# Optimization experiments

Measured on AMD Instinct MI355X. Metric: run time of the kernel, lower is better.

## Reference

```python
import jax, jax.numpy as jnp
import numpy as np

EMB = 1024
HEADS = 16
HEAD_DIM = EMB // HEADS
B, T = 2, 2048
EPS = 1e-5


def setup_inputs() -> dict:
    key = jax.random.key(0)
    ks = jax.random.split(key, 12)
    s_in = (1.0 / np.sqrt(EMB)).astype(np.float32)
    s_hid = (1.0 / np.sqrt(4 * EMB)).astype(np.float32)
    return {
        "x": jax.random.normal(ks[0], (B, T, EMB), jnp.float32),
        "Wq": jax.random.normal(ks[1], (HEADS, EMB, HEAD_DIM), jnp.float32) * s_in,
        "Wk": jax.random.normal(ks[2], (HEADS, EMB, HEAD_DIM), jnp.float32) * s_in,
        "Wv": jax.random.normal(ks[3], (HEADS, EMB, HEAD_DIM), jnp.float32) * s_in,
        "W1": jax.random.normal(ks[4], (EMB, 4 * EMB), jnp.float32) * s_in,
        "b1": jnp.zeros((4 * EMB,), jnp.float32),
        "W2": jax.random.normal(ks[5], (4 * EMB, EMB), jnp.float32) * s_hid,
        "b2": jnp.zeros((EMB,), jnp.float32),
        "g1": jnp.ones((EMB,), jnp.float32),
        "be1": jnp.zeros((EMB,), jnp.float32),
        "g2": jnp.ones((EMB,), jnp.float32),
        "be2": jnp.zeros((EMB,), jnp.float32),
    }


def _layernorm1d(x, gain, bias):
    # Faithful to source: normalize over dim 1 (sequence dim of [B,T,C]),
    # with UNBIASED variance (torch.var default).
    mean = jnp.mean(x, axis=1, keepdims=True)
    var = jnp.var(x, axis=1, keepdims=True, ddof=1)
    return gain * (x - mean) / jnp.sqrt(var + EPS) + bias


def _attention(x, Wq, Wk, Wv):
    Bq, Tq, C = x.shape
    q = jnp.einsum("btc,hcd->bhtd", x, Wq)
    k = jnp.einsum("btc,hcd->bhtd", x, Wk)
    v = jnp.einsum("btc,hcd->bhtd", x, Wv)
    # NOTE: scale uses input channel dim C (=emb_size), as in the source.
    wei = jnp.einsum("bhtd,bhsd->bhts", q, k) * (C ** -0.5)
    causal = jnp.tril(jnp.ones((Tq, Tq), bool))
    wei = jnp.where(causal, wei, -jnp.inf)
    wei = jax.nn.softmax(wei, axis=-1)
    out = jnp.einsum("bhts,bhsd->bhtd", wei, v)
    # concat over heads (dim=-1) == transpose + reshape
    return out.transpose(0, 2, 1, 3).reshape(Bq, Tq, -1)


def reference(x, Wq, Wk, Wv, W1, b1, W2, b2, g1, be1, g2, be2):
    x = x + _attention(_layernorm1d(x, g1, be1), Wq, Wk, Wv)
    h = _layernorm1d(x, g2, be2)
    h = jax.nn.relu(h @ W1 + b1) @ W2 + b2
    return x + h
```

## Files before the change

kernel.cpp:

```cpp
#include <hip/hip_runtime.h>


typedef __bf16 bf16x8 __attribute__((ext_vector_type(8)));
typedef float f32x4 __attribute__((ext_vector_type(4)));
typedef unsigned short u16;
typedef u16 u16x8 __attribute__((ext_vector_type(8)));
typedef u16 u16x4 __attribute__((ext_vector_type(4)));

#define MFMA16 __builtin_amdgcn_mfma_f32_16x16x32_bf16

__device__ __forceinline__ u16 f2bf(float f) {
  return __builtin_bit_cast(u16, (__bf16)f);
}
__device__ __forceinline__ float bf2f(u16 u) {
  return __builtin_bit_cast(float, (unsigned)u << 16);
}
__device__ __forceinline__ bf16x8 ldbf8(const u16* p) {
  return __builtin_bit_cast(bf16x8, *reinterpret_cast<const u16x8*>(p));
}
__device__ __forceinline__ void gll16(const void* g, void* l) {
  __builtin_amdgcn_global_load_lds((const __attribute__((address_space(1))) void*)g,
                                   (__attribute__((address_space(3))) void*)l, 16, 0, 0);
}
template <int N>
__device__ __forceinline__ void wait_vm() {
  if constexpr (N == 0)      asm volatile("s_waitcnt vmcnt(0)" ::: "memory");
  else if constexpr (N == 6) asm volatile("s_waitcnt vmcnt(6)" ::: "memory");
  else if constexpr (N == 8) asm volatile("s_waitcnt vmcnt(8)" ::: "memory");
  else                       asm volatile("s_waitcnt vmcnt(16)" ::: "memory");
}
__device__ __forceinline__ void barrier_raw() {
  asm volatile("" ::: "memory");
  __builtin_amdgcn_s_barrier();
  asm volatile("" ::: "memory");
}
__device__ __forceinline__ int qb_off(int qb) {
  if (qb < 8)  return qb;
  if (qb < 16) return 8 + (qb - 8) * 2;
  if (qb < 24) return 24 + (qb - 16) * 3;
  return 48 + (qb - 24) * 4;
}

__global__ __launch_bounds__(256) void transpose_big2(const float* __restrict__ W1,
                                                      const float* __restrict__ W2,
                                                      u16* __restrict__ o1,
                                                      u16* __restrict__ o2) {
  __shared__ float tile[64][65];
  int id = blockIdx.x;
  const float* in;
  u16* out;
  int K, N, kb, nb;
  if (id < 1024) { in = W1; out = o1; K = 1024; N = 4096; kb = id & 15; nb = id >> 4; }
  else { id -= 1024; in = W2; out = o2; K = 4096; N = 1024; kb = id >> 4; nb = id & 15; }
  const int k0 = kb * 64, n0 = nb * 64;
  const int c = threadIdx.x & 63, rg = threadIdx.x >> 6;
#pragma unroll
  for (int i = 0; i < 16; ++i) {
    int r = rg * 16 + i;
    tile[r][c] = in[(size_t)(k0 + r) * N + n0 + c];
  }
  __syncthreads();
#pragma unroll
  for (int i = 0; i < 16; ++i) {
    int nl = rg * 16 + i;
    out[(size_t)(n0 + nl) * K + k0 + c] = f2bf(tile[c][nl]);
  }
}

__global__ __launch_bounds__(256) void transpose_head3(const float* __restrict__ Wq,
                                                       const float* __restrict__ Wk,
                                                       const float* __restrict__ Wv,
                                                       u16* __restrict__ out, float scale) {
  __shared__ float tile[64][65];
  const int z = blockIdx.z;
  const float* W = z == 0 ? Wq : (z == 1 ? Wk : Wv);
  const float sc = z == 0 ? scale : 1.0f;
  const int k0 = blockIdx.x * 64, h = blockIdx.y;
  const float* in = W + (size_t)h * 1024 * 64;
  const int c = threadIdx.x & 63, rg = threadIdx.x >> 6;
#pragma unroll
  for (int i = 0; i < 16; ++i) {
    int r = rg * 16 + i;
    tile[r][c] = in[(size_t)(k0 + r) * 64 + c];
  }
  __syncthreads();
#pragma unroll
  for (int i = 0; i < 16; ++i) {
    int nl = rg * 16 + i;
    out[(size_t)(z * 1024 + h * 64 + nl) * 1024 + k0 + c] = f2bf(tile[c][nl] * sc);
  }
}

__global__ __launch_bounds__(256) void ln_partial(const float* __restrict__ x,
                                                  float2* __restrict__ part) {
  const int b = blockIdx.x >> 4, c0 = (blockIdx.x & 15) * 64;
  const int c = c0 + (threadIdx.x & 63), tg = threadIdx.x >> 6;
  const int t0 = blockIdx.y * 256 + tg * 64;
  float s = 0.f, sq = 0.f;
  const float* p = x + (size_t)(b * 2048 + t0) * 1024 + c;
#pragma unroll 8
  for (int i = 0; i < 64; ++i) {
    float v = p[(size_t)i * 1024];
    s += v; sq += v * v;
  }
  __shared__ float ss[256], sb[256];
  ss[threadIdx.x] = s; sb[threadIdx.x] = sq;
  __syncthreads();
  if (threadIdx.x < 64) {
    s  = ss[threadIdx.x] + ss[threadIdx.x + 64] + ss[threadIdx.x + 128] + ss[threadIdx.x + 192];
    sq = sb[threadIdx.x] + sb[threadIdx.x + 64] + sb[threadIdx.x + 128] + sb[threadIdx.x + 192];
    part[(size_t)(b * 1024 + c) * 8 + blockIdx.y] = make_float2(s, sq);
  }
}

template <int NC>
__global__ __launch_bounds__(256) void ln_stats(const float2* __restrict__ part,
                                                float2* __restrict__ stats) {
  const int bc = blockIdx.x * 256 + threadIdx.x;
  float s = 0.f, sq = 0.f;
#pragma unroll
  for (int i = 0; i < NC; ++i) {
    float2 v = part[(size_t)bc * NC + i];
    s += v.x; sq += v.y;
  }
  const float mean = s * (1.0f / 2048.0f);
  const float var = (sq - 2048.0f * mean * mean) * (1.0f / 2047.0f);
  stats[bc] = make_float2(mean, rsqrtf(var + 1e-5f));
}

__global__ __launch_bounds__(256) void ln_apply(const float* __restrict__ x,
                                                const float2* __restrict__ stats,
                                                const float* __restrict__ g,
                                                const float* __restrict__ be,
                                                u16* __restrict__ out) {
  const size_t flat = ((size_t)blockIdx.x * 256 + threadIdx.x) * 4;
  const int b = (int)(flat >> 21);
  const int c = (int)(flat & 1023);
  float4 xv = *reinterpret_cast<const float4*>(x + flat);
  float vs[4] = {xv.x, xv.y, xv.z, xv.w};
  u16x4 o;
#pragma unroll
  for (int j = 0; j < 4; ++j) {
    float2 st = stats[b * 1024 + c + j];
    o[j] = f2bf(g[c + j] * (vs[j] - st.x) * st.y + be[c + j]);
  }
  *reinterpret_cast<u16x4*>(out + flat) = o;
}

template <int WTN, int EPI, int MINW>
__global__ __launch_bounds__(256, MINW) void gemm_kernel(const u16* __restrict__ A,
                                                         const u16* __restrict__ Bt,
                                                         u16* __restrict__ outb,
                                                         float* __restrict__ outf,
                                                         const float* __restrict__ bias,
                                                         const float* __restrict__ resid,
                                                         int N, int K) {
  constexpr int BM = 128, BN = 2 * WTN;
  constexpr int NI = WTN / 16;
  constexpr int BCH = BN / 8;
  constexpr int LPW = (16 + BCH) / 4;
  __shared__ alignas(16) u16 sA[2][BM * 64];
  __shared__ alignas(16) u16 sB[2][BN * 64];
  const int gx = gridDim.x;
  const int nwg = gx * gridDim.y;
  int bid = blockIdx.y * gx + blockIdx.x;
  bid = (bid & 7) * (nwg >> 3) + (bid >> 3);
  const int n0 = (bid % gx) * BN, m0 = (bid / gx) * BM;
  const int tid = threadIdx.x, lane = tid & 63, wid = tid >> 6;
  const int wm = (wid >> 1) * 64, wn = (wid & 1) * WTN;
  const int lr = lane & 15, lg = lane >> 4;
  const int srow = lane >> 3;
  const int sgr = (lane & 7) ^ srow;
  const int x7 = lr & 7;
  f32x4 acc[4][NI] = {};

  auto stage = [&](int buf, int k0) {
#pragma unroll
    for (int i = 0; i < LPW; ++i) {
      const int c = wid * LPW + i;
      if (c < 16) {
        const int r = c * 8 + srow;
        gll16(A + (size_t)(m0 + r) * K + k0 + sgr * 8, &sA[buf][c * 512]);
      } else {
        const int r = (c - 16) * 8 + srow;
        gll16(Bt + (size_t)(n0 + r) * K + k0 + sgr * 8, &sB[buf][(c - 16) * 512]);
      }
    }
  };

  const int nsteps = K >> 6;
  stage(0, 0);
  int cur = 0;
  for (int t = 0; t < nsteps; ++t) {
    if (t + 1 < nsteps) {
      stage(cur ^ 1, (t + 1) * 64);
      wait_vm<LPW>();
    } else {
      wait_vm<0>();
    }
    barrier_raw();
    bf16x8 af[4][2], bfr[NI][2];
#pragma unroll
    for (int mi = 0; mi < 4; ++mi)
#pragma unroll
      for (int kk = 0; kk < 2; ++kk)
        af[mi][kk] = ldbf8(&sA[cur][(wm + mi * 16 + lr) * 64 + (((kk * 4 + lg) ^ x7) * 8)]);
#pragma unroll
    for (int ni = 0; ni < NI; ++ni)
#pragma unroll
      for (int kk = 0; kk < 2; ++kk)
        bfr[ni][kk] = ldbf8(&sB[cur][(wn + ni * 16 + lr) * 64 + (((kk * 4 + lg) ^ x7) * 8)]);
#pragma unroll
    for (int kk = 0; kk < 2; ++kk)
#pragma unroll
      for (int mi = 0; mi < 4; ++mi)
#pragma unroll
        for (int ni = 0; ni < NI; ++ni)
          acc[mi][ni] = MFMA16(af[mi][kk], bfr[ni][kk], acc[mi][ni], 0, 0, 0);
    barrier_raw();
    cur ^= 1;
  }

#pragma unroll
  for (int mi = 0; mi < 4; ++mi)
#pragma unroll
    for (int ni = 0; ni < NI; ++ni)
#pragma unroll
      for (int r = 0; r < 4; ++r) {
        const int row = m0 + wm + mi * 16 + lg * 4 + r;
        const int col = n0 + wn + ni * 16 + lr;
        float v = acc[mi][ni][r];
        if (EPI == 0) {
          outb[(size_t)row * N + col] = f2bf(v);
        } else if (EPI == 1) {
          v += bias[col];
          v = fmaxf(v, 0.f);
          outb[(size_t)row * N + col] = f2bf(v);
        } else {
          v += bias[col] + resid[(size_t)row * N + col];
          outf[(size_t)row * N + col] = v;
        }
      }
}

__global__ __launch_bounds__(256) void attn_partial(const u16* __restrict__ qk,
                                                    const u16* __restrict__ vt,
                                                    u16* __restrict__ Opart,
                                                    float2* __restrict__ ml) {
  const int xr = 79 - (int)blockIdx.x;
  int qb, ch, nc;
  if (xr < 8)       { qb = xr;                ch = 0;            nc = 1; }
  else if (xr < 24) { qb = 8 + ((xr - 8) >> 1);  ch = (xr - 8) & 1;  nc = 2; }
  else if (xr < 48) { qb = 16 + (xr - 24) / 3;   ch = (xr - 24) % 3; nc = 3; }
  else              { qb = 24 + ((xr - 48) >> 2); ch = (xr - 48) & 3; nc = 4; }
  const int nt_tot = qb + 1;
  const int t0 = (ch * nt_tot) / nc;
  const int t1 = ((ch + 1) * nt_tot) / nc;
  const int bh = blockIdx.y, b = bh >> 4, h = bh & 15;
  const int slot = bh * 80 + xr;
  const int q0 = qb * 64;
  const int tid = threadIdx.x, lane = tid & 63, w = tid >> 6;
  const int lr = lane & 15, lg = lane >> 4;
  __shared__ alignas(16) u16 sK[64 * 64];
  __shared__ alignas(16) u16 sV[64 * 64];
  __shared__ alignas(16) u16 sP[4][16 * 64];

  const size_t qrow = (size_t)(b * 2048 + q0 + w * 16 + lr) * 2048 + h * 64;
  const bf16x8 aq0 = ldbf8(qk + qrow + lg * 8);
  const bf16x8 aq1 = ldbf8(qk + qrow + 32 + lg * 8);

  float m_i[4], l_i[4];
  f32x4 acc[4];
#pragma unroll
  for (int r = 0; r < 4; ++r) { m_i[r] = -1e30f; l_i[r] = 0.f; }
#pragma unroll
  for (int dn = 0; dn < 4; ++dn) acc[dn] = f32x4{0.f, 0.f, 0.f, 0.f};

  auto stage = [&](int s0) {
#pragma unroll
    for (int i = 0; i < 2; ++i) {
      const int c = w * 2 + i;
      const int g = c * 64 + lane;
      const int row = g >> 3;
      const int cs = (g & 7) ^ (row & 7);
      gll16(qk + (size_t)(b * 2048 + s0 + row) * 2048 + 1024 + h * 64 + cs * 8,
            &sK[c * 512]);
      gll16(vt + (size_t)(h * 64 + row) * 4096 + b * 2048 + s0 + cs * 8,
            &sV[c * 512]);
    }
  };

  for (int t = t0; t < t1; ++t) {
    stage(t * 64);
    wait_vm<0>();
    barrier_raw();

    f32x4 sf[4];
    __builtin_amdgcn_s_setprio(1);
#pragma unroll
    for (int sn = 0; sn < 4; ++sn) {
      const int row = sn * 16 + lr;
      const int x7 = lr & 7;
      bf16x8 k0f = ldbf8(&sK[row * 64 + ((lg ^ x7) * 8)]);
      bf16x8 k1f = ldbf8(&sK[row * 64 + (((4 + lg) ^ x7) * 8)]);
      f32x4 z = {0.f, 0.f, 0.f, 0.f};
      z = MFMA16(aq0, k0f, z, 0, 0, 0);
      z = MFMA16(aq1, k1f, z, 0, 0, 0);
      sf[sn] = z;
    }
    __builtin_amdgcn_s_setprio(0);

    if (t == nt_tot - 1) {
      const int qlb = w * 16 + lg * 4;
#pragma unroll
      for (int sn = 0; sn < 4; ++sn)
#pragma unroll
        for (int r = 0; r < 4; ++r)
          if (sn * 16 + lr > qlb + r) sf[sn][r] = -1e30f;
    }

    float pm[4];
    bool need = false;
#pragma unroll
    for (int r = 0; r < 4; ++r) {
      pm[r] = fmaxf(fmaxf(sf[0][r], sf[1][r]), fmaxf(sf[2][r], sf[3][r]));
      need = need || (pm[r] > m_i[r] + 8.f);
    }
    if (__any(need)) {
#pragma unroll
      for (int r = 0; r < 4; ++r) {
        float mx = pm[r];
        mx = fmaxf(mx, __shfl_xor(mx, 1, 16));
        mx = fmaxf(mx, __shfl_xor(mx, 2, 16));
        mx = fmaxf(mx, __shfl_xor(mx, 4, 16));
        mx = fmaxf(mx, __shfl_xor(mx, 8, 16));
        const float mnew = fmaxf(m_i[r], mx);
        const float al = exp2f(m_i[r] - mnew);
        l_i[r] *= al;
        acc[0][r] *= al; acc[1][r] *= al; acc[2][r] *= al; acc[3][r] *= al;
        m_i[r] = mnew;
      }
    }

    const int x7p = lr & 7;
#pragma unroll
    for (int r = 0; r < 4; ++r) {
      const float p0 = exp2f(sf[0][r] - m_i[r]), p1 = exp2f(sf[1][r] - m_i[r]);
      const float p2 = exp2f(sf[2][r] - m_i[r]), p3 = exp2f(sf[3][r] - m_i[r]);
      l_i[r] += (p0 + p1) + (p2 + p3);
      const int prow = lg * 4 + r;
      const int pb = prow * 64, px = prow & 7;
      sP[w][pb + (((lr >> 3) ^ px) * 8) + (lr & 7)]       = f2bf(p0);
      sP[w][pb + (((2 + (lr >> 3)) ^ px) * 8) + (lr & 7)] = f2bf(p1);
      sP[w][pb + (((4 + (lr >> 3)) ^ px) * 8) + (lr & 7)] = f2bf(p2);
      sP[w][pb + (((6 + (lr >> 3)) ^ px) * 8) + (lr & 7)] = f2bf(p3);
    }

    const bf16x8 pa0 = ldbf8(&sP[w][lr * 64 + ((lg ^ x7p) * 8)]);
    const bf16x8 pa1 = ldbf8(&sP[w][lr * 64 + (((4 + lg) ^ x7p) * 8)]);
    __builtin_amdgcn_s_setprio(1);
#pragma unroll
    for (int dn = 0; dn < 4; ++dn) {
      const int row = dn * 16 + lr;
      bf16x8 v0f = ldbf8(&sV[row * 64 + ((lg ^ x7p) * 8)]);
      bf16x8 v1f = ldbf8(&sV[row * 64 + (((4 + lg) ^ x7p) * 8)]);
      acc[dn] = MFMA16(pa0, v0f, acc[dn], 0, 0, 0);
      acc[dn] = MFMA16(pa1, v1f, acc[dn], 0, 0, 0);
    }
    __builtin_amdgcn_s_setprio(0);
    barrier_raw();
  }

  const int rbase = w * 16 + lg * 4;
#pragma unroll
  for (int r = 0; r < 4; ++r) {
    float ls = l_i[r];
    ls += __shfl_xor(ls, 1, 16);
    ls += __shfl_xor(ls, 2, 16);
    ls += __shfl_xor(ls, 4, 16);
    ls += __shfl_xor(ls, 8, 16);
    const int row = rbase + r;
    if (lr == 0) ml[(size_t)slot * 64 + row] = make_float2(m_i[r], ls);
#pragma unroll
    for (int dn = 0; dn < 4; ++dn)
      Opart[((size_t)slot * 64 + row) * 64 + dn * 16 + lr] = f2bf(acc[dn][r]);
  }
}

__global__ __launch_bounds__(256) void attn_merge_ln(const u16* __restrict__ Opart,
                                                     const float2* __restrict__ ml,
                                                     const float* __restrict__ x,
                                                     float* __restrict__ x2,
                                                     float2* __restrict__ part) {
  const int qb = blockIdx.x, bh = blockIdx.y, b = bh >> 4, h = bh & 15;
  const int nc = (qb >> 3) + 1;
  const size_t slot0 = (size_t)bh * 80 + qb_off(qb);
  const int tid = threadIdx.x;
  const int row = tid >> 2, d0 = (tid & 3) * 16;
  __shared__ float red[64][65];

  float wgt[4];
  float mmax = -1e30f, lsum = 0.f;
  for (int i = 0; i < nc; ++i) {
    float2 v = ml[(slot0 + i) * 64 + row];
    wgt[i] = v.x;
    mmax = fmaxf(mmax, v.x);
  }
  for (int i = 0; i < nc; ++i) {
    float2 v = ml[(slot0 + i) * 64 + row];
    wgt[i] = exp2f(wgt[i] - mmax);
    lsum += wgt[i] * v.y;
  }
  const float inv = 1.0f / lsum;

#pragma unroll
  for (int half = 0; half < 2; ++half) {
    const int d = d0 + half * 8;
    float o[8] = {0.f, 0.f, 0.f, 0.f, 0.f, 0.f, 0.f, 0.f};
    for (int i = 0; i < nc; ++i) {
      u16x8 v = *reinterpret_cast<const u16x8*>(&Opart[((slot0 + i) * 64 + row) * 64 + d]);
#pragma unroll
      for (int jj = 0; jj < 8; ++jj) o[jj] += wgt[i] * bf2f(v[jj]);
    }
    const size_t idx = ((size_t)(b * 2048 + qb * 64 + row)) * 1024 + h * 64 + d;
    float4 x0 = *reinterpret_cast<const float4*>(x + idx);
    float4 x1 = *reinterpret_cast<const float4*>(x + idx + 4);
    float4 o0 = make_float4(x0.x + o[0] * inv, x0.y + o[1] * inv, x0.z + o[2] * inv, x0.w + o[3] * inv);
    float4 o1 = make_float4(x1.x + o[4] * inv, x1.y + o[5] * inv, x1.z + o[6] * inv, x1.w + o[7] * inv);
    *reinterpret_cast<float4*>(x2 + idx) = o0;
    *reinterpret_cast<float4*>(x2 + idx + 4) = o1;
    red[row][d + 0] = o0.x; red[row][d + 1] = o0.y; red[row][d + 2] = o0.z; red[row][d + 3] = o0.w;
    red[row][d + 4] = o1.x; red[row][d + 5] = o1.y; red[row][d + 6] = o1.z; red[row][d + 7] = o1.w;
  }
  __syncthreads();
  if (tid < 64) {
    float s = 0.f, sq = 0.f;
#pragma unroll 8
    for (int t = 0; t < 64; ++t) {
      float v = red[t][tid];
      s += v; sq += v * v;
    }
    part[(size_t)(b * 1024 + h * 64 + tid) * 32 + qb] = make_float2(s, sq);
  }
}

extern "C" void kernel_launch(void* const* d_in, const int* in_sizes, int n_in,
                              void* d_out, int out_size, void* d_ws, size_t ws_size,
                              hipStream_t stream) {
  const float* x   = (const float*)d_in[0];
  const float* Wq  = (const float*)d_in[1];
  const float* Wk  = (const float*)d_in[2];
  const float* Wv  = (const float*)d_in[3];
  const float* W1  = (const float*)d_in[4];
  const float* b1  = (const float*)d_in[5];
  const float* W2  = (const float*)d_in[6];
  const float* b2  = (const float*)d_in[7];
  const float* g1  = (const float*)d_in[8];
  const float* be1 = (const float*)d_in[9];
  const float* g2  = (const float*)d_in[10];
  const float* be2 = (const float*)d_in[11];
  float* out = (float*)d_out;

  char* ws = (char*)d_ws;
  size_t off = 0;
  auto alloc = [&](size_t bytes) { char* p = ws + off; off += (bytes + 255) & ~(size_t)255; return p; };
  u16*    qkb   = (u16*)alloc(4096ull * 2048 * 2);
  u16*    vtb   = (u16*)alloc(1024ull * 4096 * 2);
  (void)alloc(4096ull * 1024 * 2);
  u16*    h1    = qkb;
  float*  x2    = (float*)alloc(4096ull * 1024 * 4);
  u16*    hbuf  = (u16*)alloc(4096ull * 1024 * 2);
  u16*    wqkvt = (u16*)alloc(3072ull * 1024 * 2);
  u16*    w1t   = (u16*)alloc(4096ull * 1024 * 2);
  u16*    w2t   = (u16*)alloc(1024ull * 4096 * 2);
  float2* part  = (float2*)alloc(2048ull * 32 * 8);
  float2* stats = (float2*)alloc(2048ull * 8);
  u16*    Opart = (u16*)alloc(32ull * 80 * 64 * 64 * 2);
  float2* ml    = (float2*)alloc(32ull * 80 * 64 * 8);
  (void)ws_size; (void)in_sizes; (void)n_in; (void)out_size;

  const float SC = 0.03125f * 1.44269504088896341f;
  transpose_head3<<<dim3(16, 16, 3), 256, 0, stream>>>(Wq, Wk, Wv, wqkvt, SC);
  transpose_big2<<<2048, 256, 0, stream>>>(W1, W2, w1t, w2t);

  ln_partial<<<dim3(32, 8), 256, 0, stream>>>(x, part);
  ln_stats<8><<<8, 256, 0, stream>>>(part, stats);
  ln_apply<<<4096, 256, 0, stream>>>(x, stats, g1, be1, hbuf);

  gemm_kernel<64, 0, 2><<<dim3(16, 32), 256, 0, stream>>>(hbuf, wqkvt, qkb, nullptr, nullptr, nullptr, 2048, 1024);
  gemm_kernel<32, 0, 3><<<dim3(64, 8), 256, 0, stream>>>(wqkvt + 2048 * 1024, hbuf, vtb, nullptr, nullptr, nullptr, 4096, 1024);

  attn_partial<<<dim3(80, 32), 256, 0, stream>>>(qkb, vtb, Opart, ml);
  attn_merge_ln<<<dim3(32, 32), 256, 0, stream>>>(Opart, ml, x, x2, part);

  ln_stats<32><<<8, 256, 0, stream>>>(part, stats);
  ln_apply<<<4096, 256, 0, stream>>>(x2, stats, g2, be2, hbuf);

  gemm_kernel<64, 1, 2><<<dim3(32, 32), 256, 0, stream>>>(hbuf, w1t, h1, nullptr, b1, nullptr, 4096, 1024);

  gemm_kernel<32, 2, 3><<<dim3(16, 32), 256, 0, stream>>>(h1, w2t, nullptr, out, b2, x2, 1024, 4096);
}
```

Baseline: 237.4 us.

## Register-prefetch next K/V tile to overlap global loads with attention compute

Replaces the direct global-to-LDS loads, which were waited on immediately, with register-staged loads. The next K/V tile is fetched into registers while the current tile is computed, then written to LDS at the start of the next iteration. This is meant to hide global memory latency behind the QK and PV MFMA work. In exchange it uses more VGPRs, which may lower occupancy, and adds explicit LDS stores plus a restructured barrier placement.

```diff
diff --git a/kernel.cpp b/kernel.cpp
--- a/kernel.cpp
+++ b/kernel.cpp
@@ -276,23 +276,32 @@
 #pragma unroll
   for (int dn = 0; dn < 4; ++dn) acc[dn] = f32x4{0.f, 0.f, 0.f, 0.f};
 
-  auto stage = [&](int s0) {
-#pragma unroll
-    for (int i = 0; i < 2; ++i) {
-      const int c = w * 2 + i;
-      const int g = c * 64 + lane;
-      const int row = g >> 3;
-      const int cs = (g & 7) ^ (row & 7);
-      gll16(qk + (size_t)(b * 2048 + s0 + row) * 2048 + 1024 + h * 64 + cs * 8,
-            &sK[c * 512]);
-      gll16(vt + (size_t)(h * 64 + row) * 4096 + b * 2048 + s0 + cs * 8,
-            &sV[c * 512]);
-    }
+  const int c0 = w * 2, c1 = w * 2 + 1;
+  const int g0 = c0 * 64 + lane, r0 = g0 >> 3, cs0 = (g0 & 7) ^ (r0 & 7);
+  const int g1 = c1 * 64 + lane, r1 = g1 >> 3, cs1 = (g1 & 7) ^ (r1 & 7);
+  const u16* kbase0 = qk + (size_t)(b * 2048 + r0) * 2048 + 1024 + h * 64 + cs0 * 8;
+  const u16* kbase1 = qk + (size_t)(b * 2048 + r1) * 2048 + 1024 + h * 64 + cs1 * 8;
+  const u16* vbase0 = vt + (size_t)(h * 64 + r0) * 4096 + b * 2048 + cs0 * 8;
+  const u16* vbase1 = vt + (size_t)(h * 64 + r1) * 4096 + b * 2048 + cs1 * 8;
+
+  u16x8 kA0, kA1, vA0, vA1, kB0, kB1, vB0, vB1;
+  auto LOAD = [&](int s0, u16x8& k0r, u16x8& k1r, u16x8& v0r, u16x8& v1r) {
+    k0r = *reinterpret_cast<const u16x8*>(kbase0 + (size_t)s0 * 2048);
+    k1r = *reinterpret_cast<const u16x8*>(kbase1 + (size_t)s0 * 2048);
+    v0r = *reinterpret_cast<const u16x8*>(vbase0 + s0);
+    v1r = *reinterpret_cast<const u16x8*>(vbase1 + s0);
   };
 
+  LOAD(t0 * 64, kA0, kA1, vA0, vA1);
+
   for (int t = t0; t < t1; ++t) {
-    stage(t * 64);
-    wait_vm<0>();
+    barrier_raw();
+    *reinterpret_cast<u16x8*>(&sK[c0 * 512 + lane * 8]) = kA0;
+    *reinterpret_cast<u16x8*>(&sK[c1 * 512 + lane * 8]) = kA1;
+    *reinterpret_cast<u16x8*>(&sV[c0 * 512 + lane * 8]) = vA0;
+    *reinterpret_cast<u16x8*>(&sV[c1 * 512 + lane * 8]) = vA1;
+    if (t + 1 < t1) LOAD((t + 1) * 64, kB0, kB1, vB0, vB1);
+    asm volatile("s_waitcnt lgkmcnt(0)" ::: "memory");
     barrier_raw();
 
     f32x4 sf[4];
@@ -368,7 +377,8 @@
       acc[dn] = MFMA16(pa1, v1f, acc[dn], 0, 0, 0);
     }
     __builtin_amdgcn_s_setprio(0);
-    barrier_raw();
+
+    kA0 = kB0; kA1 = kB1; vA0 = vB0; vA1 = vB1;
   }
 
   const int rbase = w * 16 + lg * 4;
```

Result: slower. 243.3 us (+2.5%).

## Enlarge attention query tile to 128 rows so each K/V tile serves two halves

Applied to the files above, without the earlier changes.

Each attention block now handles 128 query rows instead of 64, with each wave owning 32 rows split into two 16-row halves. Every staged K/V tile is reused across both halves, which halves global K/V traffic and barrier count per query row. The split-KV schedule, partial-output layout, merge kernel (now 512 threads, 128 rows) and LN partial count are adjusted to match. In exchange the grid has half as many attention blocks (1280 vs 2560), register use rises, and causal masking now covers the last two KV tiles.

```diff
diff --git a/kernel.cpp b/kernel.cpp
--- a/kernel.cpp
+++ b/kernel.cpp
@@ -34,11 +34,11 @@
   __builtin_amdgcn_s_barrier();
   asm volatile("" ::: "memory");
 }
-__device__ __forceinline__ int qb_off(int qb) {
-  if (qb < 8)  return qb;
-  if (qb < 16) return 8 + (qb - 8) * 2;
-  if (qb < 24) return 24 + (qb - 16) * 3;
-  return 48 + (qb - 24) * 4;
+__device__ __forceinline__ int qb_off2(int k) {
+  if (k < 4)  return k;
+  if (k < 8)  return 4 + (k - 4) * 2;
+  if (k < 12) return 12 + (k - 8) * 3;
+  return 24 + (k - 12) * 4;
 }
 
 __global__ __launch_bounds__(256) void transpose_big2(const float* __restrict__ W1,
@@ -247,34 +247,38 @@
                                                     const u16* __restrict__ vt,
                                                     u16* __restrict__ Opart,
                                                     float2* __restrict__ ml) {
-  const int xr = 79 - (int)blockIdx.x;
-  int qb, ch, nc;
-  if (xr < 8)       { qb = xr;                ch = 0;            nc = 1; }
-  else if (xr < 24) { qb = 8 + ((xr - 8) >> 1);  ch = (xr - 8) & 1;  nc = 2; }
-  else if (xr < 48) { qb = 16 + (xr - 24) / 3;   ch = (xr - 24) % 3; nc = 3; }
-  else              { qb = 24 + ((xr - 48) >> 2); ch = (xr - 48) & 3; nc = 4; }
-  const int nt_tot = qb + 1;
+  const int xr = 39 - (int)blockIdx.x;
+  int k, ch, nc;
+  if (xr < 4)       { k = xr;                 ch = 0;             nc = 1; }
+  else if (xr < 12) { k = 4 + ((xr - 4) >> 1);   ch = (xr - 4) & 1;   nc = 2; }
+  else if (xr < 24) { k = 8 + (xr - 12) / 3;    ch = (xr - 12) % 3;  nc = 3; }
+  else              { k = 12 + ((xr - 24) >> 2); ch = (xr - 24) & 3;  nc = 4; }
+  const int nt_tot = 2 * k + 2;
   const int t0 = (ch * nt_tot) / nc;
   const int t1 = ((ch + 1) * nt_tot) / nc;
   const int bh = blockIdx.y, b = bh >> 4, h = bh & 15;
-  const int slot = bh * 80 + xr;
-  const int q0 = qb * 64;
+  const int slot = bh * 40 + xr;
+  const int q0 = k * 128;
   const int tid = threadIdx.x, lane = tid & 63, w = tid >> 6;
   const int lr = lane & 15, lg = lane >> 4;
   __shared__ alignas(16) u16 sK[64 * 64];
   __shared__ alignas(16) u16 sV[64 * 64];
-  __shared__ alignas(16) u16 sP[4][16 * 64];
-
-  const size_t qrow = (size_t)(b * 2048 + q0 + w * 16 + lr) * 2048 + h * 64;
-  const bf16x8 aq0 = ldbf8(qk + qrow + lg * 8);
-  const bf16x8 aq1 = ldbf8(qk + qrow + 32 + lg * 8);
-
-  float m_i[4], l_i[4];
-  f32x4 acc[4];
-#pragma unroll
-  for (int r = 0; r < 4; ++r) { m_i[r] = -1e30f; l_i[r] = 0.f; }
-#pragma unroll
-  for (int dn = 0; dn < 4; ++dn) acc[dn] = f32x4{0.f, 0.f, 0.f, 0.f};
+  __shared__ alignas(16) u16 sP[4][32 * 64];
+
+  const size_t qr0 = (size_t)(b * 2048 + q0 + w * 32 + lr) * 2048 + h * 64;
+  const size_t qr1 = qr0 + (size_t)16 * 2048;
+  const bf16x8 aq[2][2] = {{ldbf8(qk + qr0 + lg * 8), ldbf8(qk + qr0 + 32 + lg * 8)},
+                           {ldbf8(qk + qr1 + lg * 8), ldbf8(qk + qr1 + 32 + lg * 8)}};
+
+  float m_i[2][4], l_i[2][4];
+  f32x4 acc[2][4];
+#pragma unroll
+  for (int hf = 0; hf < 2; ++hf)
+#pragma unroll
+    for (int r = 0; r < 4; ++r) {
+      m_i[hf][r] = -1e30f; l_i[hf][r] = 0.f;
+      acc[hf][r] = f32x4{0.f, 0.f, 0.f, 0.f};
+    }
 
   auto stage = [&](int s0) {
 #pragma unroll
@@ -290,124 +294,131 @@
     }
   };
 
+  const int x7p = lr & 7;
   for (int t = t0; t < t1; ++t) {
     stage(t * 64);
     wait_vm<0>();
     barrier_raw();
 
-    f32x4 sf[4];
-    __builtin_amdgcn_s_setprio(1);
-#pragma unroll
-    for (int sn = 0; sn < 4; ++sn) {
-      const int row = sn * 16 + lr;
-      const int x7 = lr & 7;
-      bf16x8 k0f = ldbf8(&sK[row * 64 + ((lg ^ x7) * 8)]);
-      bf16x8 k1f = ldbf8(&sK[row * 64 + (((4 + lg) ^ x7) * 8)]);
-      f32x4 z = {0.f, 0.f, 0.f, 0.f};
-      z = MFMA16(aq0, k0f, z, 0, 0, 0);
-      z = MFMA16(aq1, k1f, z, 0, 0, 0);
-      sf[sn] = z;
-    }
-    __builtin_amdgcn_s_setprio(0);
-
-    if (t == nt_tot - 1) {
-      const int qlb = w * 16 + lg * 4;
-#pragma unroll
-      for (int sn = 0; sn < 4; ++sn)
-#pragma unroll
-        for (int r = 0; r < 4; ++r)
-          if (sn * 16 + lr > qlb + r) sf[sn][r] = -1e30f;
-    }
-
-    float pm[4];
-    bool need = false;
+#pragma unroll
+    for (int hf = 0; hf < 2; ++hf) {
+      f32x4 sf[4];
+      __builtin_amdgcn_s_setprio(1);
+#pragma unroll
+      for (int sn = 0; sn < 4; ++sn) {
+        const int row = sn * 16 + lr;
+        bf16x8 k0f = ldbf8(&sK[row * 64 + ((lg ^ x7p) * 8)]);
+        bf16x8 k1f = ldbf8(&sK[row * 64 + (((4 + lg) ^ x7p) * 8)]);
+        f32x4 z = {0.f, 0.f, 0.f, 0.f};
+        z = MFMA16(aq[hf][0], k0f, z, 0, 0, 0);
+        z = MFMA16(aq[hf][1], k1f, z, 0, 0, 0);
+        sf[sn] = z;
+      }
+      __builtin_amdgcn_s_setprio(0);
+
+      if (t >= nt_tot - 2) {
+        const int ds = (t - (nt_tot - 2)) * 64;
+        const int qlb = w * 32 + hf * 16 + lg * 4;
+#pragma unroll
+        for (int sn = 0; sn < 4; ++sn)
+#pragma unroll
+          for (int r = 0; r < 4; ++r)
+            if (ds + sn * 16 + lr > qlb + r) sf[sn][r] = -1e30f;
+      }
+
+      float pm[4];
+      bool need = false;
+#pragma unroll
+      for (int r = 0; r < 4; ++r) {
+        pm[r] = fmaxf(fmaxf(sf[0][r], sf[1][r]), fmaxf(sf[2][r], sf[3][r]));
+        need = need || (pm[r] > m_i[hf][r] + 8.f);
+      }
+      if (__any(need)) {
+#pragma unroll
+        for (int r = 0; r < 4; ++r) {
+          float mx = pm[r];
+          mx = fmaxf(mx, __shfl_xor(mx, 1, 16));
+          mx = fmaxf(mx, __shfl_xor(mx, 2, 16));
+          mx = fmaxf(mx, __shfl_xor(mx, 4, 16));
+          mx = fmaxf(mx, __shfl_xor(mx, 8, 16));
+          const float mnew = fmaxf(m_i[hf][r], mx);
+          const float al = exp2f(m_i[hf][r] - mnew);
+          l_i[hf][r] *= al;
+          acc[hf][r] *= al;
+          m_i[hf][r] = mnew;
+        }
+      }
+
+#pragma unroll
+      for (int r = 0; r < 4; ++r) {
+        const float p0 = exp2f(sf[0][r] - m_i[hf][r]), p1 = exp2f(sf[1][r] - m_i[hf][r]);
+        const float p2 = exp2f(sf[2][r] - m_i[hf][r]), p3 = exp2f(sf[3][r] - m_i[hf][r]);
+        l_i[hf][r] += (p0 + p1) + (p2 + p3);
+        const int prow = hf * 16 + lg * 4 + r;
+        const int pb = prow * 64, px = prow & 7;
+        sP[w][pb + (((lr >> 3) ^ px) * 8) + (lr & 7)]       = f2bf(p0);
+        sP[w][pb + (((2 + (lr >> 3)) ^ px) * 8) + (lr & 7)] = f2bf(p1);
+        sP[w][pb + (((4 + (lr >> 3)) ^ px) * 8) + (lr & 7)] = f2bf(p2);
+        sP[w][pb + (((6 + (lr >> 3)) ^ px) * 8) + (lr & 7)] = f2bf(p3);
+      }
+
+      const int pr = hf * 16 + lr;
+      const bf16x8 pa0 = ldbf8(&sP[w][pr * 64 + ((lg ^ x7p) * 8)]);
+      const bf16x8 pa1 = ldbf8(&sP[w][pr * 64 + (((4 + lg) ^ x7p) * 8)]);
+      __builtin_amdgcn_s_setprio(1);
+#pragma unroll
+      for (int dn = 0; dn < 4; ++dn) {
+        const int row = dn * 16 + lr;
+        bf16x8 v0f = ldbf8(&sV[row * 64 + ((lg ^ x7p) * 8)]);
+        bf16x8 v1f = ldbf8(&sV[row * 64 + (((4 + lg) ^ x7p) * 8)]);
+        acc[hf][dn] = MFMA16(pa0, v0f, acc[hf][dn], 0, 0, 0);
+        acc[hf][dn] = MFMA16(pa1, v1f, acc[hf][dn], 0, 0, 0);
+      }
+      __builtin_amdgcn_s_setprio(0);
+    }
+    barrier_raw();
+  }
+
+#pragma unroll
+  for (int hf = 0; hf < 2; ++hf) {
+    const int rbase = w * 32 + hf * 16 + lg * 4;
 #pragma unroll
     for (int r = 0; r < 4; ++r) {
-      pm[r] = fmaxf(fmaxf(sf[0][r], sf[1][r]), fmaxf(sf[2][r], sf[3][r]));
-      need = need || (pm[r] > m_i[r] + 8.f);
-    }
-    if (__any(need)) {
-#pragma unroll
-      for (int r = 0; r < 4; ++r) {
-        float mx = pm[r];
-        mx = fmaxf(mx, __shfl_xor(mx, 1, 16));
-        mx = fmaxf(mx, __shfl_xor(mx, 2, 16));
-        mx = fmaxf(mx, __shfl_xor(mx, 4, 16));
-        mx = fmaxf(mx, __shfl_xor(mx, 8, 16));
-        const float mnew = fmaxf(m_i[r], mx);
-        const float al = exp2f(m_i[r] - mnew);
-        l_i[r] *= al;
-        acc[0][r] *= al; acc[1][r] *= al; acc[2][r] *= al; acc[3][r] *= al;
-        m_i[r] = mnew;
-      }
-    }
-
-    const int x7p = lr & 7;
-#pragma unroll
-    for (int r = 0; r < 4; ++r) {
-      const float p0 = exp2f(sf[0][r] - m_i[r]), p1 = exp2f(sf[1][r] - m_i[r]);
-      const float p2 = exp2f(sf[2][r] - m_i[r]), p3 = exp2f(sf[3][r] - m_i[r]);
-      l_i[r] += (p0 + p1) + (p2 + p3);
-      const int prow = lg * 4 + r;
-      const int pb = prow * 64, px = prow & 7;
-      sP[w][pb + (((lr >> 3) ^ px) * 8) + (lr & 7)]       = f2bf(p0);
-      sP[w][pb + (((2 + (lr >> 3)) ^ px) * 8) + (lr & 7)] = f2bf(p1);
-      sP[w][pb + (((4 + (lr >> 3)) ^ px) * 8) + (lr & 7)] = f2bf(p2);
-      sP[w][pb + (((6 + (lr >> 3)) ^ px) * 8) + (lr & 7)] = f2bf(p3);
-    }
-
-    const bf16x8 pa0 = ldbf8(&sP[w][lr * 64 + ((lg ^ x7p) * 8)]);
-    const bf16x8 pa1 = ldbf8(&sP[w][lr * 64 + (((4 + lg) ^ x7p) * 8)]);
-    __builtin_amdgcn_s_setprio(1);
-#pragma unroll
-    for (int dn = 0; dn < 4; ++dn) {
-      const int row = dn * 16 + lr;
-      bf16x8 v0f = ldbf8(&sV[row * 64 + ((lg ^ x7p) * 8)]);
-      bf16x8 v1f = ldbf8(&sV[row * 64 + (((4 + lg) ^ x7p) * 8)]);
-      acc[dn] = MFMA16(pa0, v0f, acc[dn], 0, 0, 0);
-      acc[dn] = MFMA16(pa1, v1f, acc[dn], 0, 0, 0);
-    }
-    __builtin_amdgcn_s_setprio(0);
-    barrier_raw();
-  }
-
-  const int rbase = w * 16 + lg * 4;
-#pragma unroll
-  for (int r = 0; r < 4; ++r) {
-    float ls = l_i[r];
-    ls += __shfl_xor(ls, 1, 16);
-    ls += __shfl_xor(ls, 2, 16);
-    ls += __shfl_xor(ls, 4, 16);
-    ls += __shfl_xor(ls, 8, 16);
-    const int row = rbase + r;
-    if (lr == 0) ml[(size_t)slot * 64 + row] = make_float2(m_i[r], ls);
-#pragma unroll
-    for (int dn = 0; dn < 4; ++dn)
-      Opart[((size_t)slot * 64 + row) * 64 + dn * 16 + lr] = f2bf(acc[dn][r]);
-  }
-}
-
-__global__ __launch_bounds__(256) void attn_merge_ln(const u16* __restrict__ Opart,
+      float ls = l_i[hf][r];
+      ls += __shfl_xor(ls, 1, 16);
+      ls += __shfl_xor(ls, 2, 16);
+      ls += __shfl_xor(ls, 4, 16);
+      ls += __shfl_xor(ls, 8, 16);
+      const int row = rbase + r;
+      if (lr == 0) ml[(size_t)slot * 128 + row] = make_float2(m_i[hf][r], ls);
+#pragma unroll
+      for (int dn = 0; dn < 4; ++dn)
+        Opart[((size_t)slot * 128 + row) * 64 + dn * 16 + lr] = f2bf(acc[hf][dn][r]);
+    }
+  }
+}
+
+__global__ __launch_bounds__(512) void attn_merge_ln(const u16* __restrict__ Opart,
                                                      const float2* __restrict__ ml,
                                                      const float* __restrict__ x,
                                                      float* __restrict__ x2,
                                                      float2* __restrict__ part) {
-  const int qb = blockIdx.x, bh = blockIdx.y, b = bh >> 4, h = bh & 15;
-  const int nc = (qb >> 3) + 1;
-  const size_t slot0 = (size_t)bh * 80 + qb_off(qb);
+  const int k = blockIdx.x, bh = blockIdx.y, b = bh >> 4, h = bh & 15;
+  const int nc = (k >> 2) + 1;
+  const size_t slot0 = (size_t)bh * 40 + qb_off2(k);
   const int tid = threadIdx.x;
   const int row = tid >> 2, d0 = (tid & 3) * 16;
-  __shared__ float red[64][65];
+  __shared__ float red[128][65];
 
   float wgt[4];
   float mmax = -1e30f, lsum = 0.f;
   for (int i = 0; i < nc; ++i) {
-    float2 v = ml[(slot0 + i) * 64 + row];
+    float2 v = ml[(slot0 + i) * 128 + row];
     wgt[i] = v.x;
     mmax = fmaxf(mmax, v.x);
   }
   for (int i = 0; i < nc; ++i) {
-    float2 v = ml[(slot0 + i) * 64 + row];
+    float2 v = ml[(slot0 + i) * 128 + row];
     wgt[i] = exp2f(wgt[i] - mmax);
     lsum += wgt[i] * v.y;
   }
@@ -418,11 +429,11 @@
     const int d = d0 + half * 8;
     float o[8] = {0.f, 0.f, 0.f, 0.f, 0.f, 0.f, 0.f, 0.f};
     for (int i = 0; i < nc; ++i) {
-      u16x8 v = *reinterpret_cast<const u16x8*>(&Opart[((slot0 + i) * 64 + row) * 64 + d]);
+      u16x8 v = *reinterpret_cast<const u16x8*>(&Opart[((slot0 + i) * 128 + row) * 64 + d]);
 #pragma unroll
       for (int jj = 0; jj < 8; ++jj) o[jj] += wgt[i] * bf2f(v[jj]);
     }
-    const size_t idx = ((size_t)(b * 2048 + qb * 64 + row)) * 1024 + h * 64 + d;
+    const size_t idx = ((size_t)(b * 2048 + k * 128 + row)) * 1024 + h * 64 + d;
     float4 x0 = *reinterpret_cast<const float4*>(x + idx);
     float4 x1 = *reinterpret_cast<const float4*>(x + idx + 4);
     float4 o0 = make_float4(x0.x + o[0] * inv, x0.y + o[1] * inv, x0.z + o[2] * inv, x0.w + o[3] * inv);
@@ -436,11 +447,11 @@
   if (tid < 64) {
     float s = 0.f, sq = 0.f;
 #pragma unroll 8
-    for (int t = 0; t < 64; ++t) {
+    for (int t = 0; t < 128; ++t) {
       float v = red[t][tid];
       s += v; sq += v * v;
     }
-    part[(size_t)(b * 1024 + h * 64 + tid) * 32 + qb] = make_float2(s, sq);
+    part[(size_t)(b * 1024 + h * 64 + tid) * 16 + k] = make_float2(s, sq);
   }
 }
 
@@ -475,8 +486,8 @@
   u16*    w2t   = (u16*)alloc(1024ull * 4096 * 2);
   float2* part  = (float2*)alloc(2048ull * 32 * 8);
   float2* stats = (float2*)alloc(2048ull * 8);
-  u16*    Opart = (u16*)alloc(32ull * 80 * 64 * 64 * 2);
-  float2* ml    = (float2*)alloc(32ull * 80 * 64 * 8);
+  u16*    Opart = (u16*)alloc(32ull * 40 * 128 * 64 * 2);
+  float2* ml    = (float2*)alloc(32ull * 40 * 128 * 8);
   (void)ws_size; (void)in_sizes; (void)n_in; (void)out_size;
 
   const float SC = 0.03125f * 1.44269504088896341f;
@@ -490,10 +501,10 @@
   gemm_kernel<64, 0, 2><<<dim3(16, 32), 256, 0, stream>>>(hbuf, wqkvt, qkb, nullptr, nullptr, nullptr, 2048, 1024);
   gemm_kernel<32, 0, 3><<<dim3(64, 8), 256, 0, stream>>>(wqkvt + 2048 * 1024, hbuf, vtb, nullptr, nullptr, nullptr, 4096, 1024);
 
-  attn_partial<<<dim3(80, 32), 256, 0, stream>>>(qkb, vtb, Opart, ml);
-  attn_merge_ln<<<dim3(32, 32), 256, 0, stream>>>(Opart, ml, x, x2, part);
-
-  ln_stats<32><<<8, 256, 0, stream>>>(part, stats);
+  attn_partial<<<dim3(40, 32), 256, 0, stream>>>(qkb, vtb, Opart, ml);
+  attn_merge_ln<<<dim3(16, 32), 512, 0, stream>>>(Opart, ml, x, x2, part);
+
+  ln_stats<16><<<8, 256, 0, stream>>>(part, stats);
   ln_apply<<<4096, 256, 0, stream>>>(x2, stats, g2, be2, hbuf);
 
   gemm_kernel<64, 1, 2><<<dim3(32, 32), 256, 0, stream>>>(hbuf, w1t, h1, nullptr, b1, nullptr, 4096, 1024);
```

After: 253.3 us. 1.07x slower.
